# Kernel optimization log

Measured on AMD Instinct MI355X. Metric: run time of the kernel, lower is better.

Reference implementation:

```python
import jax, jax.numpy as jnp
import numpy as np

B, T, C, U, W = 8, 2048, 512, 512, 2


def setup_inputs() -> dict:
    key = jax.random.key(0)
    k1, k2 = jax.random.split(key)
    x = jax.random.normal(k1, (B, T, C), dtype=jnp.float32)
    # Conv1D kernel: [window, in_channels, 3*units] (z, f, o gates), glorot-ish scale
    kernel = jax.random.normal(k2, (W, C, 3 * U), dtype=jnp.float32) * (1.0 / np.sqrt(W * C))
    bias = jnp.zeros((3 * U,), dtype=jnp.float32)
    initial_state = jnp.zeros((1, U), dtype=jnp.float32)
    return {"x": x, "kernel": kernel, "bias": bias, "initial_state": initial_state}


def reference(x, kernel, bias, initial_state):
    # Causal Conv1D: pad (window-1) on the left of the time axis.
    window = kernel.shape[0]
    gates = jax.lax.conv_general_dilated(
        x, kernel,
        window_strides=(1,),
        padding=[(window - 1, 0)],
        dimension_numbers=("NWC", "WIO", "NWC"),
    ) + bias  # [B, T, 3U]
    z, f, o = jnp.split(gates, 3, axis=-1)
    z = jnp.tanh(z)
    f = jax.nn.sigmoid(f)
    o = jax.nn.sigmoid(o)

    # fo-pool recurrence: h_t = f_t * h_{t-1} + (1 - f_t) * z_t
    h0 = jnp.repeat(initial_state, x.shape[0], axis=0)  # [B, U]
    fs = jnp.moveaxis(f, 1, 0)  # [T, B, U]
    zs = jnp.moveaxis(z, 1, 0)  # [T, B, U]

    def step(h, fz):
        f_t, z_t = fz
        h = f_t * h + (1.0 - f_t) * z_t
        return h, h

    _, hs = jax.lax.scan(step, h0, (fs, zs))  # hs: [T, B, U]
    recurrent = jnp.moveaxis(hs, 0, 1)  # [B, T, U]

    # output gate, return_sequences=True
    return recurrent * o
```

## Files before the change

### kernel.cpp

```cpp
#include <hip/hip_runtime.h>


#define Bn 8
#define Tn 2048
#define Cn 512
#define Un 512
#define Nn 1536
#define Kn 1024
#define Mn (Bn * Tn)
#define NC 64
#define CL 32

using bf16x8 = __attribute__((ext_vector_type(8))) __bf16;
using f32x4  = __attribute__((ext_vector_type(4))) float;

__device__ __forceinline__ void async16(const void* g, void* l) {
  __builtin_amdgcn_global_load_lds((const __attribute__((address_space(1))) void*)g,
                                   (__attribute__((address_space(3))) void*)l, 16, 0, 0);
}

__device__ __forceinline__ unsigned short f2bf(float v) {
  union { float f; unsigned u; } c; c.f = v;
  unsigned u = c.u;
  return (unsigned short)((u + 0x7fffu + ((u >> 16) & 1u)) >> 16);
}

__device__ __forceinline__ float fast_sigmoid(float x) {
  float e = __builtin_amdgcn_exp2f(-1.4426950408889634f * x);
  return __builtin_amdgcn_rcpf(1.0f + e);
}
__device__ __forceinline__ float fast_tanh(float x) {
  float e = __builtin_amdgcn_exp2f(-2.8853900817779268f * x);
  return 2.0f * __builtin_amdgcn_rcpf(1.0f + e) - 1.0f;
}

__global__ __launch_bounds__(256) void conv_x(const float* __restrict__ x,
                                              unsigned short* __restrict__ xb) {
  int idx = blockIdx.x * 256 + threadIdx.x;
  int c4  = idx & 127;
  int row = idx >> 7;
  int b   = row / (Tn + 1);
  int t   = row - b * (Tn + 1);
  ushort4 ov;
  if (t == 0) {
    ov.x = ov.y = ov.z = ov.w = 0;
  } else {
    float4 v = *(const float4*)(x + (size_t)(b * Tn + t - 1) * Cn + c4 * 4);
    ov.x = f2bf(v.x); ov.y = f2bf(v.y); ov.z = f2bf(v.z); ov.w = f2bf(v.w);
  }
  *(ushort4*)(xb + (size_t)row * Cn + c4 * 4) = ov;
}

__global__ __launch_bounds__(256) void conv_k(const float* __restrict__ kern,
                                              unsigned short* __restrict__ kT) {
  __shared__ float tile[32][33];
  int kb = blockIdx.x, nb = blockIdx.y;
  int tx = threadIdx.x & 31, ty = threadIdx.x >> 5;
#pragma unroll
  for (int i = 0; i < 4; i++)
    tile[ty + i * 8][tx] = kern[(size_t)(kb * 32 + ty + i * 8) * Nn + nb * 32 + tx];
  __syncthreads();
#pragma unroll
  for (int i = 0; i < 4; i++) {
    int n = nb * 32 + ty + i * 8;
    int k = kb * 32 + tx;
    kT[(size_t)n * Kn + k] = f2bf(tile[tx][ty + i * 8]);
  }
}

__global__ __launch_bounds__(256) void gemm_gates(const unsigned short* __restrict__ xb,
                                                  const unsigned short* __restrict__ kT,
                                                  const float* __restrict__ bias,
                                                  float* __restrict__ gates) {
  __shared__ unsigned short As[128 * 64];
  __shared__ unsigned short Bs[128 * 64];
  const int tid = threadIdx.x;
  const int m0 = blockIdx.x * 128;
  const int n0 = blockIdx.y * 128;
  const int batch = m0 / Tn;
  const int lane = tid & 63;
  const int w = tid >> 6, wr = w >> 1, wc = w & 1;

  const int srow = (w << 3) + (lane >> 3);
  const int skq  = (lane & 7) ^ (lane >> 3);
  const unsigned short* aStage = xb + (size_t)(m0 + batch + srow) * Cn + (skq << 3);
  const unsigned short* bStage = kT + (size_t)(n0 + srow) * Kn + (skq << 3);

  f32x4 zero = {0.f, 0.f, 0.f, 0.f};
  f32x4 acc[4][4];
#pragma unroll
  for (int i = 0; i < 4; i++)
#pragma unroll
    for (int j = 0; j < 4; j++) acc[i][j] = zero;

  const int rA0 = wr * 64 + (lane & 15);
  const int rB0 = wc * 64 + (lane & 15);
  const int swz = lane & 7;

  for (int k0 = 0; k0 < Kn; k0 += 64) {
#pragma unroll
    for (int j = 0; j < 4; j++) {
      async16(aStage + (size_t)(j << 5) * Cn + k0, &As[(j * 256 + tid) * 8]);
      async16(bStage + (size_t)(j << 5) * Kn + k0, &Bs[(j * 256 + tid) * 8]);
    }
    __builtin_amdgcn_s_waitcnt(0);
    __syncthreads();

#pragma unroll
    for (int ks = 0; ks < 2; ks++) {
      const int col = (((ks << 2) + (lane >> 4)) ^ swz) << 3;
      bf16x8 af[4], bf[4];
#pragma unroll
      for (int i = 0; i < 4; i++) {
        af[i] = *(const bf16x8*)&As[(rA0 + i * 16) * 64 + col];
        bf[i] = *(const bf16x8*)&Bs[(rB0 + i * 16) * 64 + col];
      }
#pragma unroll
      for (int i = 0; i < 4; i++)
#pragma unroll
        for (int j = 0; j < 4; j++)
          acc[i][j] = __builtin_amdgcn_mfma_f32_16x16x32_bf16(af[i], bf[j], acc[i][j], 0, 0, 0);
    }
    __syncthreads();
  }

  const int region = blockIdx.y >> 2;
  const int rowB = wr * 64 + (lane >> 4) * 4;
  const int colB = wc * 64 + (lane & 15);
#pragma unroll
  for (int i = 0; i < 4; i++)
#pragma unroll
    for (int j = 0; j < 4; j++)
#pragma unroll
      for (int r = 0; r < 4; r++) {
        int mm = m0 + rowB + i * 16 + r;
        int nn = n0 + colB + j * 16;
        float g = acc[i][j][r] + bias[nn];
        float a = (region == 0) ? fast_tanh(g) : fast_sigmoid(g);
        gates[(size_t)mm * Nn + nn] = a;
      }
}

__global__ __launch_bounds__(128) void scan_phaseA(const float* __restrict__ gates,
                                                   float* __restrict__ aArr,
                                                   float* __restrict__ bArr) {
  int u4 = threadIdx.x * 4;
  int blk = blockIdx.x;
  int b = blk >> 6, c = blk & (NC - 1);
  const float* gp = gates + (size_t)(b * Tn + c * CL) * Nn;
  float4 a = {1.f, 1.f, 1.f, 1.f}, bv = {0.f, 0.f, 0.f, 0.f};
#pragma unroll 4
  for (int t = 0; t < CL; t++) {
    float4 z = *(const float4*)(gp + u4);
    float4 f = *(const float4*)(gp + Un + u4);
    a.x *= f.x; a.y *= f.y; a.z *= f.z; a.w *= f.w;
    bv.x = f.x * bv.x + (1.0f - f.x) * z.x;
    bv.y = f.y * bv.y + (1.0f - f.y) * z.y;
    bv.z = f.z * bv.z + (1.0f - f.z) * z.z;
    bv.w = f.w * bv.w + (1.0f - f.w) * z.w;
    gp += Nn;
  }
  *(float4*)(aArr + (size_t)blk * Un + u4) = a;
  *(float4*)(bArr + (size_t)blk * Un + u4) = bv;
}

__global__ __launch_bounds__(256) void scan_phaseB(const float* __restrict__ aArr,
                                                   const float* __restrict__ bArr,
                                                   const float* __restrict__ init,
                                                   float* __restrict__ hstart) {
  int idx = blockIdx.x * 256 + threadIdx.x;
  int b = idx >> 9, u = idx & (Un - 1);
  float h = init[u];
  for (int c = 0; c < NC; c++) {
    size_t offc = (size_t)(b * NC + c) * Un + u;
    hstart[offc] = h;
    h = aArr[offc] * h + bArr[offc];
  }
}

__global__ __launch_bounds__(128) void scan_phaseC(const float* __restrict__ gates,
                                                   const float* __restrict__ hstart,
                                                   float* __restrict__ out) {
  int u4 = threadIdx.x * 4;
  int blk = blockIdx.x;
  int b = blk >> 6, c = blk & (NC - 1);
  const float* gp = gates + (size_t)(b * Tn + c * CL) * Nn;
  float* op = out + (size_t)(b * Tn + c * CL) * Un;
  float4 h = *(const float4*)(hstart + (size_t)blk * Un + u4);
#pragma unroll 4
  for (int t = 0; t < CL; t++) {
    float4 z = *(const float4*)(gp + u4);
    float4 f = *(const float4*)(gp + Un + u4);
    float4 o = *(const float4*)(gp + 2 * Un + u4);
    h.x = f.x * h.x + (1.0f - f.x) * z.x;
    h.y = f.y * h.y + (1.0f - f.y) * z.y;
    h.z = f.z * h.z + (1.0f - f.z) * z.z;
    h.w = f.w * h.w + (1.0f - f.w) * z.w;
    float4 ov;
    ov.x = h.x * o.x; ov.y = h.y * o.y; ov.z = h.z * o.z; ov.w = h.w * o.w;
    *(float4*)(op + u4) = ov;
    gp += Nn;
    op += Un;
  }
}

extern "C" void kernel_launch(void* const* d_in, const int* in_sizes, int n_in,
                              void* d_out, int out_size, void* d_ws, size_t ws_size,
                              hipStream_t stream) {
  const float* x    = (const float*)d_in[0];
  const float* kern = (const float*)d_in[1];
  const float* bias = (const float*)d_in[2];
  const float* init = (const float*)d_in[3];
  float* out = (float*)d_out;

  char* ws = (char*)d_ws;
  unsigned short* xb = (unsigned short*)ws;
  size_t off = (size_t)Bn * (Tn + 1) * Cn * 2;
  unsigned short* kT = (unsigned short*)(ws + off);
  off += (size_t)Nn * Kn * 2;
  float* gates = (float*)(ws + off);
  off += (size_t)Mn * Nn * 4;
  float* aArr = (float*)(ws + off);  off += (size_t)Bn * NC * Un * 4;
  float* bArr = (float*)(ws + off);  off += (size_t)Bn * NC * Un * 4;
  float* hstart = (float*)(ws + off);

  conv_x<<<(Bn * (Tn + 1) * Cn / 4) / 256, 256, 0, stream>>>(x, xb);
  conv_k<<<dim3(32, 48), 256, 0, stream>>>(kern, kT);
  gemm_gates<<<dim3(Mn / 128, Nn / 128), 256, 0, stream>>>(xb, kT, bias, gates);
  scan_phaseA<<<Bn * NC, 128, 0, stream>>>(gates, aArr, bArr);
  scan_phaseB<<<(Bn * Un) / 256, 256, 0, stream>>>(aArr, bArr, init, hstart);
  scan_phaseC<<<Bn * NC, 128, 0, stream>>>(gates, hstart, out);
}
```

Measured before the change: 187.7 us.

## Store activated gates as bf16 and rework scan chunking and thread mapping

The GEMM epilogue now writes the activated gate values as bf16 instead of fp32, which halves the traffic for the large gates buffer on both the write and the two scan-pass reads. Scan phases A and C switch from float4 per thread to one unit per thread with 256-thread blocks. Chunks become 64 steps long, 32 per sequence, which keeps the same block count. The risk is lower precision in z, f and o feeding the recurrence, and scalar 2-byte loads that may coalesce less well.

Measured after the change: 175.8 us. 1.07x faster.

```diff
diff --git a/kernel.cpp b/kernel.cpp
--- a/kernel.cpp
+++ b/kernel.cpp
@@ -8,8 +8,8 @@
 #define Nn 1536
 #define Kn 1024
 #define Mn (Bn * Tn)
-#define NC 64
-#define CL 32
+#define NC 32
+#define CL 64
 
 using bf16x8 = __attribute__((ext_vector_type(8))) __bf16;
 using f32x4  = __attribute__((ext_vector_type(4))) float;
@@ -23,6 +23,11 @@
   union { float f; unsigned u; } c; c.f = v;
   unsigned u = c.u;
   return (unsigned short)((u + 0x7fffu + ((u >> 16) & 1u)) >> 16);
+}
+
+__device__ __forceinline__ float bf2f(unsigned short h) {
+  union { unsigned u; float f; } c; c.u = ((unsigned)h) << 16;
+  return c.f;
 }
 
 __device__ __forceinline__ float fast_sigmoid(float x) {
@@ -71,7 +76,7 @@
 __global__ __launch_bounds__(256) void gemm_gates(const unsigned short* __restrict__ xb,
                                                   const unsigned short* __restrict__ kT,
                                                   const float* __restrict__ bias,
-                                                  float* __restrict__ gates) {
+                                                  unsigned short* __restrict__ gates) {
   __shared__ unsigned short As[128 * 64];
   __shared__ unsigned short Bs[128 * 64];
   const int tid = threadIdx.x;
@@ -137,31 +142,28 @@
         int nn = n0 + colB + j * 16;
         float g = acc[i][j][r] + bias[nn];
         float a = (region == 0) ? fast_tanh(g) : fast_sigmoid(g);
-        gates[(size_t)mm * Nn + nn] = a;
+        gates[(size_t)mm * Nn + nn] = f2bf(a);
       }
 }
 
-__global__ __launch_bounds__(128) void scan_phaseA(const float* __restrict__ gates,
+__global__ __launch_bounds__(256) void scan_phaseA(const unsigned short* __restrict__ gates,
                                                    float* __restrict__ aArr,
                                                    float* __restrict__ bArr) {
-  int u4 = threadIdx.x * 4;
-  int blk = blockIdx.x;
-  int b = blk >> 6, c = blk & (NC - 1);
-  const float* gp = gates + (size_t)(b * Tn + c * CL) * Nn;
-  float4 a = {1.f, 1.f, 1.f, 1.f}, bv = {0.f, 0.f, 0.f, 0.f};
+  int chunk = blockIdx.x >> 1;
+  int u = (blockIdx.x & 1) * 256 + threadIdx.x;
+  int b = chunk >> 5, c = chunk & (NC - 1);
+  const unsigned short* gp = gates + (size_t)(b * Tn + c * CL) * Nn;
+  float a = 1.0f, bv = 0.0f;
 #pragma unroll 4
   for (int t = 0; t < CL; t++) {
-    float4 z = *(const float4*)(gp + u4);
-    float4 f = *(const float4*)(gp + Un + u4);
-    a.x *= f.x; a.y *= f.y; a.z *= f.z; a.w *= f.w;
-    bv.x = f.x * bv.x + (1.0f - f.x) * z.x;
-    bv.y = f.y * bv.y + (1.0f - f.y) * z.y;
-    bv.z = f.z * bv.z + (1.0f - f.z) * z.z;
-    bv.w = f.w * bv.w + (1.0f - f.w) * z.w;
+    float z = bf2f(gp[u]);
+    float f = bf2f(gp[Un + u]);
+    a *= f;
+    bv = f * bv + (1.0f - f) * z;
     gp += Nn;
   }
-  *(float4*)(aArr + (size_t)blk * Un + u4) = a;
-  *(float4*)(bArr + (size_t)blk * Un + u4) = bv;
+  aArr[(size_t)chunk * Un + u] = a;
+  bArr[(size_t)chunk * Un + u] = bv;
 }
 
 __global__ __launch_bounds__(256) void scan_phaseB(const float* __restrict__ aArr,
@@ -178,27 +180,22 @@
   }
 }
 
-__global__ __launch_bounds__(128) void scan_phaseC(const float* __restrict__ gates,
+__global__ __launch_bounds__(256) void scan_phaseC(const unsigned short* __restrict__ gates,
                                                    const float* __restrict__ hstart,
                                                    float* __restrict__ out) {
-  int u4 = threadIdx.x * 4;
-  int blk = blockIdx.x;
-  int b = blk >> 6, c = blk & (NC - 1);
-  const float* gp = gates + (size_t)(b * Tn + c * CL) * Nn;
+  int chunk = blockIdx.x >> 1;
+  int u = (blockIdx.x & 1) * 256 + threadIdx.x;
+  int b = chunk >> 5, c = chunk & (NC - 1);
+  const unsigned short* gp = gates + (size_t)(b * Tn + c * CL) * Nn;
   float* op = out + (size_t)(b * Tn + c * CL) * Un;
-  float4 h = *(const float4*)(hstart + (size_t)blk * Un + u4);
+  float h = hstart[(size_t)chunk * Un + u];
 #pragma unroll 4
   for (int t = 0; t < CL; t++) {
-    float4 z = *(const float4*)(gp + u4);
-    float4 f = *(const float4*)(gp + Un + u4);
-    float4 o = *(const float4*)(gp + 2 * Un + u4);
-    h.x = f.x * h.x + (1.0f - f.x) * z.x;
-    h.y = f.y * h.y + (1.0f - f.y) * z.y;
-    h.z = f.z * h.z + (1.0f - f.z) * z.z;
-    h.w = f.w * h.w + (1.0f - f.w) * z.w;
-    float4 ov;
-    ov.x = h.x * o.x; ov.y = h.y * o.y; ov.z = h.z * o.z; ov.w = h.w * o.w;
-    *(float4*)(op + u4) = ov;
+    float z = bf2f(gp[u]);
+    float f = bf2f(gp[Un + u]);
+    float o = bf2f(gp[2 * Un + u]);
+    h = f * h + (1.0f - f) * z;
+    op[u] = h * o;
     gp += Nn;
     op += Un;
   }
@@ -218,8 +215,8 @@
   size_t off = (size_t)Bn * (Tn + 1) * Cn * 2;
   unsigned short* kT = (unsigned short*)(ws + off);
   off += (size_t)Nn * Kn * 2;
-  float* gates = (float*)(ws + off);
-  off += (size_t)Mn * Nn * 4;
+  unsigned short* gates = (unsigned short*)(ws + off);
+  off += (size_t)Mn * Nn * 2;
   float* aArr = (float*)(ws + off);  off += (size_t)Bn * NC * Un * 4;
   float* bArr = (float*)(ws + off);  off += (size_t)Bn * NC * Un * 4;
   float* hstart = (float*)(ws + off);
@@ -227,7 +224,7 @@
   conv_x<<<(Bn * (Tn + 1) * Cn / 4) / 256, 256, 0, stream>>>(x, xb);
   conv_k<<<dim3(32, 48), 256, 0, stream>>>(kern, kT);
   gemm_gates<<<dim3(Mn / 128, Nn / 128), 256, 0, stream>>>(xb, kT, bias, gates);
-  scan_phaseA<<<Bn * NC, 128, 0, stream>>>(gates, aArr, bArr);
+  scan_phaseA<<<Bn * NC * 2, 256, 0, stream>>>(gates, aArr, bArr);
   scan_phaseB<<<(Bn * Un) / 256, 256, 0, stream>>>(aArr, bArr, init, hstart);
-  scan_phaseC<<<Bn * NC, 128, 0, stream>>>(gates, hstart, out);
-}
+  scan_phaseC<<<Bn * NC * 2, 256, 0, stream>>>(gates, hstart, out);
+}
```
